# Optimization experiments

Measured on AMD Instinct MI355X. Metric: run time of the kernel, lower is better.

Reference implementation:

```python
import jax, jax.numpy as jnp
import numpy as np

TEMP = 0.7
ALPHA_ADV = 1.0
BETA_BAND = 0.5
BAND_L = 0.05
BAND_H = 0.2
W_HEUR = 0.5
W_LEAR = 0.5


def setup_inputs() -> dict:
    key = jax.random.key(0)
    ks = jax.random.split(key, 6)
    B, Sn, C, H, W = 2, 5, 64, 192, 192
    hid = 64
    return {
        "S": jax.random.normal(ks[0], (B, C, H, W), jnp.float32),
        "T": jax.random.normal(ks[1], (B, Sn, C, H, W), jnp.float32),
        "adapt_w": jax.random.normal(ks[2], (Sn, C, C), jnp.float32) / np.sqrt(C).astype(np.float32),
        "adapt_b": jnp.zeros((Sn, C), jnp.float32),
        "r_w1": jax.random.normal(ks[3], (hid, Sn * C * 3), jnp.float32) * 0.05,
        "r_b1": jnp.zeros((hid,), jnp.float32),
        "r_w2": jax.random.normal(ks[4], (Sn, hid), jnp.float32) * 0.05,
        "r_b2": jnp.zeros((Sn,), jnp.float32),
        "ema_mu": jnp.zeros((1, Sn, C, 1, 1), jnp.float32),
        "ema_sigma": jnp.ones((1, Sn, C, 1, 1), jnp.float32),
        "ema_proxy": jnp.zeros((1, Sn, 1, 1, 1), jnp.float32),
    }


def reference(S, T, adapt_w, adapt_b, r_w1, r_b1, r_w2, r_b2, ema_mu, ema_sigma, ema_proxy):
    B, Sn, C, H, W = T.shape
    bias = adapt_b[None, :, :, None, None]
    # per-sweep 1x1 conv == per-sweep channel matmul
    T_adapt = jnp.einsum('sdc,bschw->bsdhw', adapt_w, T) + bias          # [B,S,C,H,W]
    S_rep = jnp.einsum('sdc,bchw->bsdhw', adapt_w, S) + bias             # [B,S,C,H,W]
    Tz = (T_adapt - ema_mu) / ema_sigma
    Sz = (S_rep - ema_mu) / ema_sigma
    delta = Tz - Sz
    proxy = jnp.mean(delta * delta, axis=2, keepdims=True)               # [B,S,1,H,W]
    cur = jnp.mean(proxy, axis=(0, 3, 4), keepdims=True)                 # [1,S,1,1,1]
    # heuristic score (gamma_ucb = 0 -> no UCB term)
    impr = jax.lax.stop_gradient(ema_proxy - cur)
    adv = impr - jnp.mean(impr, axis=1, keepdims=True)
    below = jnp.maximum(BAND_L - cur, 0.0)
    above = jnp.maximum(cur - BAND_H, 0.0)
    band = -(below * below + above * above)
    score = ALPHA_ADV * adv + BETA_BAND * band                           # [1,S,1,1,1]
    score_heur = jnp.broadcast_to(score, proxy.shape)[:, :, 0]           # [B,S,H,W]
    # learned router: concat along channel of each sweep then 1x1 MLP
    x = jnp.concatenate([Sz, Tz, delta], axis=2).reshape(B, Sn * 3 * C, H, W)
    h = jax.nn.relu(jnp.einsum('oi,bihw->bohw', r_w1, x) + r_b1[None, :, None, None])
    score_learn = jnp.einsum('oi,bihw->bohw', r_w2, h) + r_b2[None, :, None, None]
    logits = W_HEUR * score_heur + W_LEAR * score_learn                  # [B,S,H,W]
    weights = jax.nn.softmax(logits / TEMP, axis=1)                      # soft gating over sweeps
    return weights
```

## Files before the change

kernel.cpp:

```cpp
#include <hip/hip_runtime.h>
#include <math.h>

#define HWSZ 36864
#define NBLK3 576
#define TPX  128

typedef short bf16x8 __attribute__((ext_vector_type(8)));
typedef float f32x16 __attribute__((ext_vector_type(16)));
typedef unsigned int u32x4 __attribute__((ext_vector_type(4)));

__device__ __forceinline__ unsigned short f2bf(float x) {
    unsigned u = __float_as_uint(x);
    return (unsigned short)((u + 0x7fffu + ((u >> 16) & 1u)) >> 16);
}

__global__ void pre_weights(const float* __restrict__ rw1, const float* __restrict__ rb1,
                            const float* __restrict__ aw, const float* __restrict__ ab,
                            const float* __restrict__ mu, const float* __restrict__ sg,
                            float* __restrict__ Dmat, float* __restrict__ MT,
                            float* __restrict__ MSp, float* __restrict__ c1) {
    int idx = blockIdx.x * 256 + threadIdx.x;
    if (idx < 20480) {
        Dmat[idx] = aw[idx] / sg[idx >> 6];
        int s = idx / 4096, r = idx % 4096, o = r >> 6, c = r & 63;
        float sum = 0.f;
        const float* wp = rw1 + o * 960 + s * 192;
        const float* A  = aw + s * 4096 + c;
        const float* G  = sg + s * 64;
        #pragma unroll 8
        for (int d = 0; d < 64; ++d)
            sum = fmaf(wp[64 + d] + wp[128 + d], A[d * 64] / G[d], sum);
        MT[idx] = sum;
    } else if (idx < 24576) {
        int k = idx - 20480;
        int o = k >> 6, c = k & 63;
        float sum = 0.f;
        for (int s = 0; s < 5; ++s) {
            const float* wp = rw1 + o * 960 + s * 192;
            const float* A  = aw + s * 4096 + c;
            const float* G  = sg + s * 64;
            #pragma unroll 8
            for (int d = 0; d < 64; ++d)
                sum = fmaf(wp[d] + wp[64 + d], A[d * 64] / G[d], sum);
        }
        MSp[k] = sum;
    } else if (idx < 24640) {
        int o = idx - 24576;
        float sum = rb1[o];
        for (int s = 0; s < 5; ++s) {
            const float* wp = rw1 + o * 960 + s * 192;
            #pragma unroll 8
            for (int d = 0; d < 64; ++d) {
                int sd = s * 64 + d;
                sum = fmaf(wp[d] + wp[64 + d], (ab[sd] - mu[sd]) / sg[sd], sum);
            }
        }
        c1[o] = sum;
    }
}

__global__ void pre_pack(const float* __restrict__ Dmat, const float* __restrict__ MT,
                         const float* __restrict__ MSp,
                         unsigned short* __restrict__ AfragW,
                         unsigned short* __restrict__ AfragSp) {
    int i = blockIdx.x * 256 + threadIdx.x;
    if (i < 40960) {
        int s = i / 8192, rem = i % 8192;
        int r = rem / 2048, rem2 = rem % 2048;
        int t = rem2 / 512, q = rem2 % 512;
        int l = q >> 3, e = q & 7;
        int R = 32 * r + (l & 31);
        int k = 16 * t + 8 * (l >> 5) + e;
        float v = (R < 64) ? Dmat[s * 4096 + R * 64 + k] : MT[s * 4096 + (R - 64) * 64 + k];
        AfragW[i] = f2bf(v);
    } else if (i < 45056) {
        int j = i - 40960;
        int r = j / 2048, rem2 = j % 2048;
        int t = rem2 / 512, q = rem2 % 512;
        int l = q >> 3, e = q & 7;
        float v = MSp[(32 * r + (l & 31)) * 64 + 16 * t + 8 * (l >> 5) + e];
        AfragSp[j] = f2bf(v);
    }
}

__global__ __launch_bounds__(256, 2) void fused_main(
        const float* __restrict__ S, const float* __restrict__ T,
        const unsigned short* __restrict__ AfragW, const unsigned short* __restrict__ AfragSp,
        const float* __restrict__ c1, const float* __restrict__ rw2, const float* __restrict__ rb2,
        float* __restrict__ slearn, float* __restrict__ partial) {
    __shared__ __align__(16) unsigned short bufA[8192];
    __shared__ __align__(16) unsigned short bufB[8192];
    __shared__ float hpart[2][5][128];
    __shared__ float wred[5][2];
    __shared__ float w2s[320];
    __shared__ float c1s[64];
    __shared__ float rb2s[8];

    const int tid = threadIdx.x;
    const int lane = tid & 63;
    const int w = tid >> 6;
    const int hi = lane >> 5;
    const int pxl = lane & 31;
    const int blk = blockIdx.x;
    const int b = blk / 288;
    const int pix0 = (blk % 288) * TPX;

    const int c8 = tid >> 5;
    const int q  = tid & 31;
    const int kt8 = c8 >> 1, hh = c8 & 1;
    const float* Sp = S + ((size_t)(b * 64 + 8 * c8)) * HWSZ + pix0 + 4 * q;
    const float* Tp = T + ((size_t)(b * 5 * 64) + 8 * c8) * HWSZ + pix0 + 4 * q;

    float4 R[8];
    #pragma unroll
    for (int j = 0; j < 8; ++j) R[j] = *(const float4*)(Sp + (size_t)j * HWSZ);

    bf16x8 wf[20];
    {
        const bf16x8* afw = (const bf16x8*)AfragW + lane;
        #pragma unroll
        for (int s = 0; s < 5; ++s)
            #pragma unroll
            for (int kt = 0; kt < 4; ++kt)
                wf[s * 4 + kt] = afw[(((s * 4) + w) * 4 + kt) * 64];
    }
    bf16x8 spf[4];
    if (w >= 2) {
        const bf16x8* asp = (const bf16x8*)AfragSp + lane;
        #pragma unroll
        for (int kt = 0; kt < 4; ++kt) spf[kt] = asp[((w - 2) * 4 + kt) * 64];
    }

    for (int i = tid; i < 320; i += 256) w2s[i] = rw2[i];
    if (tid < 64) c1s[tid] = c1[tid];
    if (tid < 5)  rb2s[tid] = rb2[tid];

    unsigned swd[4][4];
    #pragma unroll
    for (int pi = 0; pi < 4; ++pi)
        #pragma unroll
        for (int e2 = 0; e2 < 4; ++e2) {
            float a = ((const float*)&R[2 * e2])[pi];
            float c = ((const float*)&R[2 * e2 + 1])[pi];
            swd[pi][e2] = (unsigned)f2bf(a) | ((unsigned)f2bf(c) << 16);
        }
    #pragma unroll
    for (int pi = 0; pi < 4; ++pi) {
        int p = 4 * q + pi;
        unsigned short* dst = &bufA[((((p >> 5) << 2) + kt8) << 9) + ((hh << 5) + (p & 31)) * 8];
        u32x4 o; o.x = swd[pi][0]; o.y = swd[pi][1]; o.z = swd[pi][2]; o.w = swd[pi][3];
        *(u32x4*)dst = o;
    }

    #pragma unroll
    for (int j = 0; j < 8; ++j) R[j] = *(const float4*)(Tp + (size_t)j * HWSZ);
    __syncthreads();

    f32x16 acc[4];
    #pragma unroll
    for (int n = 0; n < 4; ++n)
        #pragma unroll
        for (int i = 0; i < 16; ++i) acc[n][i] = 0.f;

    if (w >= 2) {
        #pragma unroll
        for (int n = 0; n < 4; ++n)
            #pragma unroll
            for (int kt = 0; kt < 4; ++kt) {
                bf16x8 Bq = *(const bf16x8*)&bufA[(((n << 2) + kt) << 9) + lane * 8];
                acc[n] = __builtin_amdgcn_mfma_f32_32x32x16_bf16(spf[kt], Bq, acc[n], 0, 0, 0);
            }
    }

    auto writeX = [&](unsigned short* buf) {
        #pragma unroll
        for (int pi = 0; pi < 4; ++pi) {
            int p = 4 * q + pi;
            unsigned o[4];
            #pragma unroll
            for (int e2 = 0; e2 < 4; ++e2) {
                unsigned sv = swd[pi][e2];
                float s0 = __uint_as_float(sv << 16);
                float s1 = __uint_as_float(sv & 0xffff0000u);
                float t0 = ((const float*)&R[2 * e2])[pi];
                float t1 = ((const float*)&R[2 * e2 + 1])[pi];
                o[e2] = (unsigned)f2bf(t0 - s0) | ((unsigned)f2bf(t1 - s1) << 16);
            }
            unsigned short* dst = &buf[((((p >> 5) << 2) + kt8) << 9) + ((hh << 5) + (p & 31)) * 8];
            u32x4 ov; ov.x = o[0]; ov.y = o[1]; ov.z = o[2]; ov.w = o[3];
            *(u32x4*)dst = ov;
        }
    };
    auto loadT = [&](int s) {
        const float* p = Tp + (size_t)(s * 64) * HWSZ;
        #pragma unroll
        for (int j = 0; j < 8; ++j) R[j] = *(const float4*)(p + (size_t)j * HWSZ);
    };

    writeX(bufB);
    loadT(1);
    __syncthreads();

    #pragma unroll
    for (int s = 0; s < 5; ++s) {
        const unsigned short* cb = (s & 1) ? bufA : bufB;
        unsigned short* nb = (s & 1) ? bufB : bufA;
        if (w < 2) {
            #pragma unroll
            for (int n = 0; n < 4; ++n)
                #pragma unroll
                for (int i = 0; i < 16; ++i) acc[n][i] = 0.f;
        }
        #pragma unroll
        for (int n = 0; n < 4; ++n)
            #pragma unroll
            for (int kt = 0; kt < 4; ++kt) {
                bf16x8 Bq = *(const bf16x8*)&cb[(((n << 2) + kt) << 9) + lane * 8];
                acc[n] = __builtin_amdgcn_mfma_f32_32x32x16_bf16(wf[s * 4 + kt], Bq, acc[n], 0, 0, 0);
            }
        if (s < 4) {
            writeX(nb);
            if (s < 3) loadT(s + 2);
        }
        if (w < 2) {
            float sq = 0.f;
            #pragma unroll
            for (int n = 0; n < 4; ++n)
                #pragma unroll
                for (int i = 0; i < 16; ++i) sq = fmaf(acc[n][i], acc[n][i], sq);
            #pragma unroll
            for (int m = 1; m < 64; m <<= 1) sq += __shfl_xor(sq, m, 64);
            if (lane == 0) wred[s][w] = sq;
        }
        __syncthreads();
    }

    if (w >= 2) {
        #pragma unroll
        for (int n = 0; n < 4; ++n)
            #pragma unroll
            for (int i = 0; i < 16; ++i) {
                int row = (i & 3) + 8 * (i >> 2) + 4 * hi + 32 * (w - 2);
                acc[n][i] = fmaxf(acc[n][i] + c1s[row], 0.f);
            }
        #pragma unroll
        for (int sp = 0; sp < 5; ++sp)
            #pragma unroll
            for (int n = 0; n < 4; ++n) {
                float dot = 0.f;
                #pragma unroll
                for (int i = 0; i < 16; ++i) {
                    int row = (i & 3) + 8 * (i >> 2) + 4 * hi + 32 * (w - 2);
                    dot = fmaf(w2s[sp * 64 + row], acc[n][i], dot);
                }
                dot += __shfl_xor(dot, 32, 64);
                if (hi == 0) hpart[w - 2][sp][n * 32 + pxl] = dot;
            }
    }
    __syncthreads();

    if (tid < 5) partial[blk * 5 + tid] = wred[tid][0] + wred[tid][1];
    for (int i = tid; i < 640; i += 256) {
        int sp = i >> 7, px = i & 127;
        slearn[((size_t)(b * 5 + sp)) * HWSZ + pix0 + px] =
            hpart[0][sp][px] + hpart[1][sp][px] + rb2s[sp];
    }
}

__global__ void score_kernel(const float* __restrict__ partial,
                             const float* __restrict__ ema_proxy,
                             float* __restrict__ scoreBuf) {
    __shared__ float red[256];
    __shared__ float cur[5];
    int tid = threadIdx.x;
    for (int s = 0; s < 5; ++s) {
        float sum = 0.f;
        for (int i = tid; i < NBLK3; i += 256) sum += partial[i * 5 + s];
        red[tid] = sum;
        __syncthreads();
        for (int off = 128; off > 0; off >>= 1) {
            if (tid < off) red[tid] += red[tid + off];
            __syncthreads();
        }
        if (tid == 0) cur[s] = red[0] * (1.0f / (64.0f * 2.0f * HWSZ));
        __syncthreads();
    }
    if (tid == 0) {
        float impr[5]; float m = 0.f;
        for (int s = 0; s < 5; ++s) { impr[s] = ema_proxy[s] - cur[s]; m += impr[s]; }
        m *= 0.2f;
        for (int s = 0; s < 5; ++s) {
            float adv = impr[s] - m;
            float c = cur[s];
            float below = fmaxf(0.05f - c, 0.f);
            float above = fmaxf(c - 0.2f, 0.f);
            float band = -(below * below + above * above);
            scoreBuf[s] = 1.0f * adv + 0.5f * band;
        }
    }
}

__global__ void softmax_kernel(const float* __restrict__ slearn,
                               const float* __restrict__ scoreBuf,
                               float* __restrict__ out) {
    int i = blockIdx.x * 256 + threadIdx.x;
    if (i >= 2 * HWSZ) return;
    int b = i / HWSZ, p = i % HWSZ;
    float l[5];
    float mx = -1e30f;
    #pragma unroll
    for (int s = 0; s < 5; ++s) {
        float v = (0.5f * scoreBuf[s] + 0.5f * slearn[((size_t)(b * 5 + s)) * HWSZ + p]) / 0.7f;
        l[s] = v;
        mx = fmaxf(mx, v);
    }
    float sum = 0.f;
    #pragma unroll
    for (int s = 0; s < 5; ++s) { l[s] = expf(l[s] - mx); sum += l[s]; }
    float inv = 1.0f / sum;
    #pragma unroll
    for (int s = 0; s < 5; ++s) out[((size_t)(b * 5 + s)) * HWSZ + p] = l[s] * inv;
}

extern "C" void kernel_launch(void* const* d_in, const int* in_sizes, int n_in,
                              void* d_out, int out_size, void* d_ws, size_t ws_size,
                              hipStream_t stream) {
    const float* S   = (const float*)d_in[0];
    const float* T   = (const float*)d_in[1];
    const float* aw  = (const float*)d_in[2];
    const float* ab  = (const float*)d_in[3];
    const float* rw1 = (const float*)d_in[4];
    const float* rb1 = (const float*)d_in[5];
    const float* rw2 = (const float*)d_in[6];
    const float* rb2 = (const float*)d_in[7];
    const float* mu  = (const float*)d_in[8];
    const float* sg  = (const float*)d_in[9];
    const float* ep  = (const float*)d_in[10];

    float* ws = (float*)d_ws;
    float* c1f      = ws;
    float* scoreBuf = ws + 64;
    float* partial  = ws + 72;
    unsigned short* AfragW  = (unsigned short*)(ws + 11592);
    unsigned short* AfragSp = (unsigned short*)(ws + 32072);
    float* slearn   = ws + 34120;
    float* Dmat     = ws + 34120;
    float* MT       = ws + 54600;
    float* MSp      = ws + 75080;
    float* out = (float*)d_out;

    pre_weights<<<97, 256, 0, stream>>>(rw1, rb1, aw, ab, mu, sg, Dmat, MT, MSp, c1f);
    pre_pack<<<176, 256, 0, stream>>>(Dmat, MT, MSp, AfragW, AfragSp);
    fused_main<<<NBLK3, 256, 0, stream>>>(S, T, AfragW, AfragSp, c1f, rw2, rb2, slearn, partial);
    score_kernel<<<1, 256, 0, stream>>>(partial, ep, scoreBuf);
    softmax_kernel<<<288, 256, 0, stream>>>(slearn, scoreBuf, out);
}
```

Baseline: 63.43 us.

## Halve pixel tile, raise occupancy, fuse weight prep, compute delta via MFMA subtraction

The main kernel now handles 64 pixels per block instead of 128, doubling the block count to 1152, and declares 4 blocks per CU instead of 2. Per-sweep weight fragments are streamed with double-buffered registers rather than all 20 being held at once. Delta is no longer computed elementwise on the host-side of the MFMA: it comes from a negated S product plus a T product, and the router's S term is folded algebraically (wp[d]-wp[128+d]). The two weight-prep kernels merge into one launch that writes the packed bf16 fragments directly, and an XOR swizzle is applied to the LDS layout. The intent is lower register pressure, better latency hiding and fewer launches, at the cost of extra MFMA work on the delta path and more partial sums to reduce.

```diff
diff --git a/kernel.cpp b/kernel.cpp
--- a/kernel.cpp
+++ b/kernel.cpp
@@ -2,8 +2,7 @@
 #include <math.h>
 
 #define HWSZ 36864
-#define NBLK3 576
-#define TPX  128
+#define NBLK4 1152
 
 typedef short bf16x8 __attribute__((ext_vector_type(8)));
 typedef float f32x16 __attribute__((ext_vector_type(16)));
@@ -14,55 +13,18 @@
     return (unsigned short)((u + 0x7fffu + ((u >> 16) & 1u)) >> 16);
 }
 
-__global__ void pre_weights(const float* __restrict__ rw1, const float* __restrict__ rb1,
-                            const float* __restrict__ aw, const float* __restrict__ ab,
-                            const float* __restrict__ mu, const float* __restrict__ sg,
-                            float* __restrict__ Dmat, float* __restrict__ MT,
-                            float* __restrict__ MSp, float* __restrict__ c1) {
-    int idx = blockIdx.x * 256 + threadIdx.x;
-    if (idx < 20480) {
-        Dmat[idx] = aw[idx] / sg[idx >> 6];
-        int s = idx / 4096, r = idx % 4096, o = r >> 6, c = r & 63;
-        float sum = 0.f;
-        const float* wp = rw1 + o * 960 + s * 192;
-        const float* A  = aw + s * 4096 + c;
-        const float* G  = sg + s * 64;
-        #pragma unroll 8
-        for (int d = 0; d < 64; ++d)
-            sum = fmaf(wp[64 + d] + wp[128 + d], A[d * 64] / G[d], sum);
-        MT[idx] = sum;
-    } else if (idx < 24576) {
-        int k = idx - 20480;
-        int o = k >> 6, c = k & 63;
-        float sum = 0.f;
-        for (int s = 0; s < 5; ++s) {
-            const float* wp = rw1 + o * 960 + s * 192;
-            const float* A  = aw + s * 4096 + c;
-            const float* G  = sg + s * 64;
-            #pragma unroll 8
-            for (int d = 0; d < 64; ++d)
-                sum = fmaf(wp[d] + wp[64 + d], A[d * 64] / G[d], sum);
-        }
-        MSp[k] = sum;
-    } else if (idx < 24640) {
-        int o = idx - 24576;
-        float sum = rb1[o];
-        for (int s = 0; s < 5; ++s) {
-            const float* wp = rw1 + o * 960 + s * 192;
-            #pragma unroll 8
-            for (int d = 0; d < 64; ++d) {
-                int sd = s * 64 + d;
-                sum = fmaf(wp[d] + wp[64 + d], (ab[sd] - mu[sd]) / sg[sd], sum);
-            }
-        }
-        c1[o] = sum;
-    }
-}
-
-__global__ void pre_pack(const float* __restrict__ Dmat, const float* __restrict__ MT,
-                         const float* __restrict__ MSp,
-                         unsigned short* __restrict__ AfragW,
-                         unsigned short* __restrict__ AfragSp) {
+__device__ __forceinline__ void block_sync_lds() {
+    __builtin_amdgcn_sched_barrier(0);
+    asm volatile("s_waitcnt lgkmcnt(0)" ::: "memory");
+    __builtin_amdgcn_s_barrier();
+    __builtin_amdgcn_sched_barrier(0);
+}
+
+__global__ void pre_all(const float* __restrict__ rw1, const float* __restrict__ rb1,
+                        const float* __restrict__ aw, const float* __restrict__ ab,
+                        const float* __restrict__ mu, const float* __restrict__ sg,
+                        unsigned short* __restrict__ AfragW,
+                        unsigned short* __restrict__ AfragMS2, float* __restrict__ c1) {
     int i = blockIdx.x * 256 + threadIdx.x;
     if (i < 40960) {
         int s = i / 8192, rem = i % 8192;
@@ -71,197 +33,215 @@
         int l = q >> 3, e = q & 7;
         int R = 32 * r + (l & 31);
         int k = 16 * t + 8 * (l >> 5) + e;
-        float v = (R < 64) ? Dmat[s * 4096 + R * 64 + k] : MT[s * 4096 + (R - 64) * 64 + k];
+        float v;
+        if (R < 64) {
+            v = aw[s * 4096 + R * 64 + k] / sg[s * 64 + R];
+        } else {
+            int o = R - 64;
+            const float* wp = rw1 + o * 960 + s * 192;
+            const float* A  = aw + s * 4096 + k;
+            const float* G  = sg + s * 64;
+            float sum = 0.f;
+            #pragma unroll 8
+            for (int d = 0; d < 64; ++d)
+                sum = fmaf(wp[64 + d] + wp[128 + d], A[d * 64] / G[d], sum);
+            v = sum;
+        }
         AfragW[i] = f2bf(v);
     } else if (i < 45056) {
         int j = i - 40960;
         int r = j / 2048, rem2 = j % 2048;
         int t = rem2 / 512, q = rem2 % 512;
         int l = q >> 3, e = q & 7;
-        float v = MSp[(32 * r + (l & 31)) * 64 + 16 * t + 8 * (l >> 5) + e];
-        AfragSp[j] = f2bf(v);
-    }
-}
-
-__global__ __launch_bounds__(256, 2) void fused_main(
+        int o = 32 * r + (l & 31);
+        int k = 16 * t + 8 * (l >> 5) + e;
+        float sum = 0.f;
+        for (int s = 0; s < 5; ++s) {
+            const float* wp = rw1 + o * 960 + s * 192;
+            const float* A  = aw + s * 4096 + k;
+            const float* G  = sg + s * 64;
+            #pragma unroll 8
+            for (int d = 0; d < 64; ++d)
+                sum = fmaf(wp[d] - wp[128 + d], A[d * 64] / G[d], sum);
+        }
+        AfragMS2[j] = f2bf(sum);
+    } else if (i < 45120) {
+        int o = i - 45056;
+        float sum = rb1[o];
+        for (int s = 0; s < 5; ++s) {
+            const float* wp = rw1 + o * 960 + s * 192;
+            #pragma unroll 8
+            for (int d = 0; d < 64; ++d) {
+                int sd = s * 64 + d;
+                sum = fmaf(wp[d] + wp[64 + d], (ab[sd] - mu[sd]) / sg[sd], sum);
+            }
+        }
+        c1[o] = sum;
+    }
+}
+
+__global__ __launch_bounds__(256, 4) void fused_main(
         const float* __restrict__ S, const float* __restrict__ T,
-        const unsigned short* __restrict__ AfragW, const unsigned short* __restrict__ AfragSp,
+        const unsigned short* __restrict__ AfragW, const unsigned short* __restrict__ AfragMS2,
         const float* __restrict__ c1, const float* __restrict__ rw2, const float* __restrict__ rb2,
         float* __restrict__ slearn, float* __restrict__ partial) {
-    __shared__ __align__(16) unsigned short bufA[8192];
-    __shared__ __align__(16) unsigned short bufB[8192];
-    __shared__ float hpart[2][5][128];
+    __shared__ __align__(16) unsigned short sTile[4096];
+    __shared__ __align__(16) unsigned short tbuf[2][4096];
+    __shared__ float hpart[2][5][64];
     __shared__ float wred[5][2];
     __shared__ float w2s[320];
     __shared__ float c1s[64];
     __shared__ float rb2s[8];
 
-    const int tid = threadIdx.x;
-    const int lane = tid & 63;
-    const int w = tid >> 6;
-    const int hi = lane >> 5;
-    const int pxl = lane & 31;
+    const int tid = threadIdx.x, lane = tid & 63, w = tid >> 6;
+    const int hi = lane >> 5, pxm = lane & 31;
     const int blk = blockIdx.x;
-    const int b = blk / 288;
-    const int pix0 = (blk % 288) * TPX;
-
-    const int c8 = tid >> 5;
-    const int q  = tid & 31;
-    const int kt8 = c8 >> 1, hh = c8 & 1;
-    const float* Sp = S + ((size_t)(b * 64 + 8 * c8)) * HWSZ + pix0 + 4 * q;
-    const float* Tp = T + ((size_t)(b * 5 * 64) + 8 * c8) * HWSZ + pix0 + 4 * q;
-
-    float4 R[8];
-    #pragma unroll
-    for (int j = 0; j < 8; ++j) R[j] = *(const float4*)(Sp + (size_t)j * HWSZ);
-
-    bf16x8 wf[20];
-    {
-        const bf16x8* afw = (const bf16x8*)AfragW + lane;
-        #pragma unroll
-        for (int s = 0; s < 5; ++s)
-            #pragma unroll
-            for (int kt = 0; kt < 4; ++kt)
-                wf[s * 4 + kt] = afw[(((s * 4) + w) * 4 + kt) * 64];
-    }
-    bf16x8 spf[4];
-    if (w >= 2) {
-        const bf16x8* asp = (const bf16x8*)AfragSp + lane;
-        #pragma unroll
-        for (int kt = 0; kt < 4; ++kt) spf[kt] = asp[((w - 2) * 4 + kt) * 64];
-    }
+    const int b = blk / 576;
+    const int pix0 = (blk % 576) * 64;
+
+    const int o8 = tid >> 5, q = tid & 31;
+    const int skt = o8 >> 1, shh = o8 & 1;
+    const float* Sp = S + ((size_t)(b * 64 + 8 * o8)) * HWSZ + pix0 + 2 * q;
+    const float* Tp = T + ((size_t)(b * 5 * 64 + 8 * o8)) * HWSZ + pix0 + 2 * q;
+
+    float2 R[8];
+    #pragma unroll
+    for (int j = 0; j < 8; ++j) R[j] = *(const float2*)(Sp + (size_t)j * HWSZ);
 
     for (int i = tid; i < 320; i += 256) w2s[i] = rw2[i];
     if (tid < 64) c1s[tid] = c1[tid];
     if (tid < 5)  rb2s[tid] = rb2[tid];
 
-    unsigned swd[4][4];
-    #pragma unroll
-    for (int pi = 0; pi < 4; ++pi)
-        #pragma unroll
-        for (int e2 = 0; e2 < 4; ++e2) {
-            float a = ((const float*)&R[2 * e2])[pi];
-            float c = ((const float*)&R[2 * e2 + 1])[pi];
-            swd[pi][e2] = (unsigned)f2bf(a) | ((unsigned)f2bf(c) << 16);
-        }
-    #pragma unroll
-    for (int pi = 0; pi < 4; ++pi) {
-        int p = 4 * q + pi;
-        unsigned short* dst = &bufA[((((p >> 5) << 2) + kt8) << 9) + ((hh << 5) + (p & 31)) * 8];
-        u32x4 o; o.x = swd[pi][0]; o.y = swd[pi][1]; o.z = swd[pi][2]; o.w = swd[pi][3];
-        *(u32x4*)dst = o;
-    }
-
-    #pragma unroll
-    for (int j = 0; j < 8; ++j) R[j] = *(const float4*)(Tp + (size_t)j * HWSZ);
-    __syncthreads();
-
-    f32x16 acc[4];
-    #pragma unroll
-    for (int n = 0; n < 4; ++n)
-        #pragma unroll
-        for (int i = 0; i < 16; ++i) acc[n][i] = 0.f;
-
+    auto packWrite = [&](unsigned short* dst) {
+        #pragma unroll
+        for (int h2 = 0; h2 < 2; ++h2) {
+            int px = 2 * q + h2;
+            int ct = px >> 5, slot = (px & 31) ^ ct;
+            u32x4 v;
+            #pragma unroll
+            for (int jj = 0; jj < 4; ++jj) {
+                float a = h2 ? R[2 * jj].y : R[2 * jj].x;
+                float c = h2 ? R[2 * jj + 1].y : R[2 * jj + 1].x;
+                v[jj] = (unsigned)f2bf(a) | ((unsigned)f2bf(c) << 16);
+            }
+            *(u32x4*)&dst[(((ct * 4 + skt) * 64) + shh * 32 + slot) * 8] = v;
+        }
+    };
+
+    packWrite(sTile);
+
+    #pragma unroll
+    for (int j = 0; j < 8; ++j) R[j] = *(const float2*)(Tp + (size_t)j * HWSZ);
+
+    const bf16x8* afw = (const bf16x8*)AfragW + lane;
+    bf16x8 fr0[4], fr1[4];
+    #pragma unroll
+    for (int kt = 0; kt < 4; ++kt) fr0[kt] = afw[((0 * 4 + w) * 4 + kt) * 64];
+    bf16x8 ms2f[4];
     if (w >= 2) {
-        #pragma unroll
-        for (int n = 0; n < 4; ++n)
+        const bf16x8* am = (const bf16x8*)AfragMS2 + lane;
+        #pragma unroll
+        for (int kt = 0; kt < 4; ++kt) ms2f[kt] = am[((w - 2) * 4 + kt) * 64];
+    }
+
+    block_sync_lds();
+
+    auto ldsB = [&](const unsigned short* buf, int ct, int kt) -> bf16x8 {
+        return *(const bf16x8*)&buf[(((ct * 4 + kt) * 64) + hi * 32 + (pxm ^ ct)) * 8];
+    };
+
+    f32x16 acc0, acc1;
+    #pragma unroll
+    for (int i = 0; i < 16; ++i) { acc0[i] = 0.f; acc1[i] = 0.f; }
+
+    if (w >= 2) {
+        #pragma unroll
+        for (int kt = 0; kt < 4; ++kt) {
+            acc0 = __builtin_amdgcn_mfma_f32_32x32x16_bf16(ms2f[kt], ldsB(sTile, 0, kt), acc0, 0, 0, 0);
+            acc1 = __builtin_amdgcn_mfma_f32_32x32x16_bf16(ms2f[kt], ldsB(sTile, 1, kt), acc1, 0, 0, 0);
+        }
+    }
+
+    packWrite(tbuf[0]);
+    #pragma unroll
+    for (int j = 0; j < 8; ++j) R[j] = *(const float2*)(Tp + (size_t)(64 + j) * HWSZ);
+
+    block_sync_lds();
+
+    #pragma unroll
+    for (int s = 0; s < 5; ++s) {
+        const unsigned short* cur = tbuf[s & 1];
+        unsigned short* nxt = tbuf[(s + 1) & 1];
+        bf16x8* fcur = (s & 1) ? fr1 : fr0;
+        bf16x8* fnxt = (s & 1) ? fr0 : fr1;
+        if (s < 4) {
+            #pragma unroll
+            for (int kt = 0; kt < 4; ++kt) fnxt[kt] = afw[(((s + 1) * 4 + w) * 4 + kt) * 64];
+        }
+        if (w < 2) {
+            #pragma unroll
+            for (int i = 0; i < 16; ++i) { acc0[i] = 0.f; acc1[i] = 0.f; }
             #pragma unroll
             for (int kt = 0; kt < 4; ++kt) {
-                bf16x8 Bq = *(const bf16x8*)&bufA[(((n << 2) + kt) << 9) + lane * 8];
-                acc[n] = __builtin_amdgcn_mfma_f32_32x32x16_bf16(spf[kt], Bq, acc[n], 0, 0, 0);
-            }
-    }
-
-    auto writeX = [&](unsigned short* buf) {
-        #pragma unroll
-        for (int pi = 0; pi < 4; ++pi) {
-            int p = 4 * q + pi;
-            unsigned o[4];
-            #pragma unroll
-            for (int e2 = 0; e2 < 4; ++e2) {
-                unsigned sv = swd[pi][e2];
-                float s0 = __uint_as_float(sv << 16);
-                float s1 = __uint_as_float(sv & 0xffff0000u);
-                float t0 = ((const float*)&R[2 * e2])[pi];
-                float t1 = ((const float*)&R[2 * e2 + 1])[pi];
-                o[e2] = (unsigned)f2bf(t0 - s0) | ((unsigned)f2bf(t1 - s1) << 16);
-            }
-            unsigned short* dst = &buf[((((p >> 5) << 2) + kt8) << 9) + ((hh << 5) + (p & 31)) * 8];
-            u32x4 ov; ov.x = o[0]; ov.y = o[1]; ov.z = o[2]; ov.w = o[3];
-            *(u32x4*)dst = ov;
-        }
-    };
-    auto loadT = [&](int s) {
-        const float* p = Tp + (size_t)(s * 64) * HWSZ;
-        #pragma unroll
-        for (int j = 0; j < 8; ++j) R[j] = *(const float4*)(p + (size_t)j * HWSZ);
-    };
-
-    writeX(bufB);
-    loadT(1);
-    __syncthreads();
-
-    #pragma unroll
-    for (int s = 0; s < 5; ++s) {
-        const unsigned short* cb = (s & 1) ? bufA : bufB;
-        unsigned short* nb = (s & 1) ? bufB : bufA;
-        if (w < 2) {
-            #pragma unroll
-            for (int n = 0; n < 4; ++n)
-                #pragma unroll
-                for (int i = 0; i < 16; ++i) acc[n][i] = 0.f;
-        }
-        #pragma unroll
-        for (int n = 0; n < 4; ++n)
+                acc0 = __builtin_amdgcn_mfma_f32_32x32x16_bf16(fcur[kt], ldsB(sTile, 0, kt), acc0, 0, 0, 0);
+                acc1 = __builtin_amdgcn_mfma_f32_32x32x16_bf16(fcur[kt], ldsB(sTile, 1, kt), acc1, 0, 0, 0);
+            }
+            #pragma unroll
+            for (int i = 0; i < 16; ++i) { acc0[i] = -acc0[i]; acc1[i] = -acc1[i]; }
             #pragma unroll
             for (int kt = 0; kt < 4; ++kt) {
-                bf16x8 Bq = *(const bf16x8*)&cb[(((n << 2) + kt) << 9) + lane * 8];
-                acc[n] = __builtin_amdgcn_mfma_f32_32x32x16_bf16(wf[s * 4 + kt], Bq, acc[n], 0, 0, 0);
-            }
-        if (s < 4) {
-            writeX(nb);
-            if (s < 3) loadT(s + 2);
-        }
-        if (w < 2) {
+                acc0 = __builtin_amdgcn_mfma_f32_32x32x16_bf16(fcur[kt], ldsB(cur, 0, kt), acc0, 0, 0, 0);
+                acc1 = __builtin_amdgcn_mfma_f32_32x32x16_bf16(fcur[kt], ldsB(cur, 1, kt), acc1, 0, 0, 0);
+            }
             float sq = 0.f;
             #pragma unroll
-            for (int n = 0; n < 4; ++n)
-                #pragma unroll
-                for (int i = 0; i < 16; ++i) sq = fmaf(acc[n][i], acc[n][i], sq);
+            for (int i = 0; i < 16; ++i) { sq = fmaf(acc0[i], acc0[i], sq); sq = fmaf(acc1[i], acc1[i], sq); }
             #pragma unroll
             for (int m = 1; m < 64; m <<= 1) sq += __shfl_xor(sq, m, 64);
             if (lane == 0) wred[s][w] = sq;
-        }
-        __syncthreads();
+        } else {
+            #pragma unroll
+            for (int kt = 0; kt < 4; ++kt) {
+                acc0 = __builtin_amdgcn_mfma_f32_32x32x16_bf16(fcur[kt], ldsB(cur, 0, kt), acc0, 0, 0, 0);
+                acc1 = __builtin_amdgcn_mfma_f32_32x32x16_bf16(fcur[kt], ldsB(cur, 1, kt), acc1, 0, 0, 0);
+            }
+        }
+        if (s < 4) {
+            packWrite(nxt);
+            if (s < 3) {
+                #pragma unroll
+                for (int j = 0; j < 8; ++j)
+                    R[j] = *(const float2*)(Tp + (size_t)((s + 2) * 64 + j) * HWSZ);
+            }
+        }
+        block_sync_lds();
     }
 
     if (w >= 2) {
         #pragma unroll
-        for (int n = 0; n < 4; ++n)
+        for (int i = 0; i < 16; ++i) {
+            int row = (i & 3) + 8 * (i >> 2) + 4 * hi + 32 * (w - 2);
+            acc0[i] = fmaxf(acc0[i] + c1s[row], 0.f);
+            acc1[i] = fmaxf(acc1[i] + c1s[row], 0.f);
+        }
+        #pragma unroll
+        for (int sp = 0; sp < 5; ++sp) {
+            float d0 = 0.f, d1 = 0.f;
             #pragma unroll
             for (int i = 0; i < 16; ++i) {
                 int row = (i & 3) + 8 * (i >> 2) + 4 * hi + 32 * (w - 2);
-                acc[n][i] = fmaxf(acc[n][i] + c1s[row], 0.f);
-            }
-        #pragma unroll
-        for (int sp = 0; sp < 5; ++sp)
-            #pragma unroll
-            for (int n = 0; n < 4; ++n) {
-                float dot = 0.f;
-                #pragma unroll
-                for (int i = 0; i < 16; ++i) {
-                    int row = (i & 3) + 8 * (i >> 2) + 4 * hi + 32 * (w - 2);
-                    dot = fmaf(w2s[sp * 64 + row], acc[n][i], dot);
-                }
-                dot += __shfl_xor(dot, 32, 64);
-                if (hi == 0) hpart[w - 2][sp][n * 32 + pxl] = dot;
-            }
-    }
-    __syncthreads();
-
+                d0 = fmaf(w2s[sp * 64 + row], acc0[i], d0);
+                d1 = fmaf(w2s[sp * 64 + row], acc1[i], d1);
+            }
+            d0 += __shfl_xor(d0, 32, 64);
+            d1 += __shfl_xor(d1, 32, 64);
+            if (hi == 0) { hpart[w - 2][sp][pxm] = d0; hpart[w - 2][sp][32 + pxm] = d1; }
+        }
+    }
+    block_sync_lds();
     if (tid < 5) partial[blk * 5 + tid] = wred[tid][0] + wred[tid][1];
-    for (int i = tid; i < 640; i += 256) {
-        int sp = i >> 7, px = i & 127;
+    for (int i = tid; i < 320; i += 256) {
+        int sp = i >> 6, px = i & 63;
         slearn[((size_t)(b * 5 + sp)) * HWSZ + pix0 + px] =
             hpart[0][sp][px] + hpart[1][sp][px] + rb2s[sp];
     }
@@ -275,7 +255,7 @@
     int tid = threadIdx.x;
     for (int s = 0; s < 5; ++s) {
         float sum = 0.f;
-        for (int i = tid; i < NBLK3; i += 256) sum += partial[i * 5 + s];
+        for (int i = tid; i < NBLK4; i += 256) sum += partial[i * 5 + s];
         red[tid] = sum;
         __syncthreads();
         for (int off = 128; off > 0; off >>= 1) {
@@ -341,17 +321,13 @@
     float* c1f      = ws;
     float* scoreBuf = ws + 64;
     float* partial  = ws + 72;
-    unsigned short* AfragW  = (unsigned short*)(ws + 11592);
-    unsigned short* AfragSp = (unsigned short*)(ws + 32072);
-    float* slearn   = ws + 34120;
-    float* Dmat     = ws + 34120;
-    float* MT       = ws + 54600;
-    float* MSp      = ws + 75080;
+    unsigned short* AfragW   = (unsigned short*)(ws + 5832);
+    unsigned short* AfragMS2 = (unsigned short*)(ws + 26312);
+    float* slearn   = ws + 28360;
     float* out = (float*)d_out;
 
-    pre_weights<<<97, 256, 0, stream>>>(rw1, rb1, aw, ab, mu, sg, Dmat, MT, MSp, c1f);
-    pre_pack<<<176, 256, 0, stream>>>(Dmat, MT, MSp, AfragW, AfragSp);
-    fused_main<<<NBLK3, 256, 0, stream>>>(S, T, AfragW, AfragSp, c1f, rw2, rb2, slearn, partial);
+    pre_all<<<177, 256, 0, stream>>>(rw1, rb1, aw, ab, mu, sg, AfragW, AfragMS2, c1f);
+    fused_main<<<NBLK4, 256, 0, stream>>>(S, T, AfragW, AfragMS2, c1f, rw2, rb2, slearn, partial);
     score_kernel<<<1, 256, 0, stream>>>(partial, ep, scoreBuf);
     softmax_kernel<<<288, 256, 0, stream>>>(slearn, scoreBuf, out);
 }
```

After: 56.11 us (median of 2 runs). 11.5% less time.
